# Kernel optimization log

Hardware: AMD Instinct MI355X
Metric: run time of the kernel (lower is better)

## Reference

```python
import jax, jax.numpy as jnp
import numpy as np

N = 50000        # nodes
E = 800000       # random edges (self loops appended inside reference, per PyG default)
IN = 128         # in_channels
H1, C1 = 8, 64   # conv1: heads, hidden_channels
NUM_CLASSES = 2  # conv2 out (heads=1, concat=False)
NEG_SLOPE = 0.2  # PyG GATConv default LeakyReLU slope


def setup_inputs() -> dict:
    key = jax.random.key(0)
    ks = jax.random.split(key, 12)
    x = jax.random.normal(ks[0], (N, IN), dtype=jnp.float32)
    edge_index = jax.random.randint(ks[1], (2, E), 0, N)
    # conv1 params: W1 [IN, H1*C1], att vectors [H1, C1], bias [H1*C1]
    W1 = jax.random.normal(ks[2], (IN, H1 * C1), dtype=jnp.float32) / np.sqrt(IN)
    a_src1 = jax.random.normal(ks[3], (H1, C1), dtype=jnp.float32) / np.sqrt(C1)
    a_dst1 = jax.random.normal(ks[4], (H1, C1), dtype=jnp.float32) / np.sqrt(C1)
    b1 = jnp.zeros((H1 * C1,), dtype=jnp.float32)
    # conv2 params: heads=1, out=NUM_CLASSES
    W2 = jax.random.normal(ks[5], (H1 * C1, 1 * NUM_CLASSES), dtype=jnp.float32) / np.sqrt(H1 * C1)
    a_src2 = jax.random.normal(ks[6], (1, NUM_CLASSES), dtype=jnp.float32) / np.sqrt(NUM_CLASSES)
    a_dst2 = jax.random.normal(ks[7], (1, NUM_CLASSES), dtype=jnp.float32) / np.sqrt(NUM_CLASSES)
    b2 = jnp.zeros((NUM_CLASSES,), dtype=jnp.float32)
    return {"x": x, "edge_index": edge_index, "W1": W1, "a_src1": a_src1,
            "a_dst1": a_dst1, "b1": b1, "W2": W2, "a_src2": a_src2,
            "a_dst2": a_dst2, "b2": b2}


def gat_layer(x, src, dst, W, a_src, a_dst, bias, concat):
    n = x.shape[0]
    heads, ch = a_src.shape
    h = (x @ W).reshape(n, heads, ch)                      # [N,H,C]
    alpha_s = jnp.einsum('nhc,hc->nh', h, a_src)           # per-node src score
    alpha_d = jnp.einsum('nhc,hc->nh', h, a_dst)           # per-node dst score
    e = jax.nn.leaky_relu(alpha_s[src] + alpha_d[dst], NEG_SLOPE)  # [Etot,H]
    # segment softmax over edges grouped by destination node
    m = jax.ops.segment_max(e, dst, num_segments=n)
    ex = jnp.exp(e - m[dst])
    den = jax.ops.segment_sum(ex, dst, num_segments=n)
    alpha = ex / den[dst]                                  # [Etot,H]
    out = jax.ops.segment_sum(h[src] * alpha[:, :, None], dst, num_segments=n)  # [N,H,C]
    out = out.reshape(n, heads * ch) if concat else out.mean(axis=1)
    return out + bias


def reference(x, edge_index, W1, a_src1, a_dst1, b1, W2, a_src2, a_dst2, b2):
    n = x.shape[0]
    loops = jnp.arange(n, dtype=edge_index.dtype)
    src = jnp.concatenate([edge_index[0], loops])   # PyG add_self_loops=True
    dst = jnp.concatenate([edge_index[1], loops])
    h = gat_layer(x, src, dst, W1, a_src1, a_dst1, b1, concat=True)   # [N, H1*C1]
    h = jax.nn.elu(h)
    # dropout is identity in eval mode
    out = gat_layer(h, src, dst, W2, a_src2, a_dst2, b2, concat=False)  # [N, 2]
    return out
```

## Files before the change

### kernel.cpp

```cpp
#include <hip/hip_runtime.h>
#include <hip/hip_bf16.h>

#define NEG 0.2f
#define BKT 64

typedef __attribute__((ext_vector_type(8))) short bf16x8;
typedef __attribute__((ext_vector_type(4))) float f32x4;

static __device__ __forceinline__ unsigned short f2bf(float f) {
    union { float f; unsigned u; } v; v.f = f;
    unsigned r = v.u + 0x7fff + ((v.u >> 16) & 1);
    return (unsigned short)(r >> 16);
}
static __device__ __forceinline__ float bf_lo(unsigned u) {
    return __uint_as_float(u << 16);
}
static __device__ __forceinline__ float bf_hi(unsigned u) {
    return __uint_as_float(u & 0xffff0000u);
}

__global__ void k_init(int* __restrict__ deg, unsigned short* __restrict__ csr, int n) {
    int v = blockIdx.x * 256 + threadIdx.x;
    if (v >= n) return;
    deg[v] = 1;
    csr[(size_t)v * BKT] = (unsigned short)v;
}

__global__ __launch_bounds__(256) void k_big(const int* __restrict__ ei,
                                             int* __restrict__ deg,
                                             unsigned short* __restrict__ csr,
                                             const float* __restrict__ x,
                                             const float* __restrict__ W1,
                                             const float* __restrict__ a_src,
                                             const float* __restrict__ a_dst,
                                             unsigned short* __restrict__ h1b,
                                             float* __restrict__ as1,
                                             float* __restrict__ ad1,
                                             int E_, int n, int gblocks) {
    int tid = threadIdx.x;
    if ((int)blockIdx.x >= gblocks) {
        int e = (blockIdx.x - gblocks) * 256 + tid;
        if (e >= E_) return;
        int s = ei[e], d = ei[E_ + e];
        int slot = atomicAdd(&deg[d], 1);
        if (slot < BKT) csr[(size_t)d * BKT + slot] = (unsigned short)s;
        return;
    }
    __shared__ unsigned short stg[4][16][72];
    int wave = tid >> 6, lane = tid & 63;
    int l15 = lane & 15, q = lane >> 4;
    int rowblk = blockIdx.x * 256 + wave * 64;

    bf16x8 xf[4][4];
    #pragma unroll
    for (int st = 0; st < 4; st++) {
        int ar = rowblk + st * 16 + l15; if (ar > n - 1) ar = n - 1;
        const float* ap = x + (size_t)ar * 128 + q * 8;
        #pragma unroll
        for (int kb = 0; kb < 4; kb++) {
            float4 v0 = *(const float4*)(ap + kb * 32);
            float4 v1 = *(const float4*)(ap + kb * 32 + 4);
            xf[st][kb][0] = (short)f2bf(v0.x); xf[st][kb][1] = (short)f2bf(v0.y);
            xf[st][kb][2] = (short)f2bf(v0.z); xf[st][kb][3] = (short)f2bf(v0.w);
            xf[st][kb][4] = (short)f2bf(v1.x); xf[st][kb][5] = (short)f2bf(v1.y);
            xf[st][kb][6] = (short)f2bf(v1.z); xf[st][kb][7] = (short)f2bf(v1.w);
        }
    }

    for (int j = 0; j < 8; j++) {
        int col0 = j * 64;
        bf16x8 bfr[4][4];
        #pragma unroll
        for (int kb = 0; kb < 4; kb++)
            #pragma unroll
            for (int t = 0; t < 4; t++) {
                const float* wp = W1 + (size_t)(kb * 32 + q * 8) * 512 + col0 + t * 16 + l15;
                #pragma unroll
                for (int e = 0; e < 8; e++)
                    bfr[kb][t][e] = (short)f2bf(wp[(size_t)e * 512]);
            }
        float asv[4], adv[4];
        #pragma unroll
        for (int t = 0; t < 4; t++) {
            asv[t] = a_src[j * 64 + t * 16 + l15];
            adv[t] = a_dst[j * 64 + t * 16 + l15];
        }

        #pragma unroll
        for (int st = 0; st < 4; st++) {
            int row0 = rowblk + st * 16;
            f32x4 acc[4] = {};
            #pragma unroll
            for (int kb = 0; kb < 4; kb++)
                #pragma unroll
                for (int t = 0; t < 4; t++)
                    acc[t] = __builtin_amdgcn_mfma_f32_16x16x32_bf16(xf[st][kb], bfr[kb][t], acc[t], 0, 0, 0);
            #pragma unroll
            for (int t = 0; t < 4; t++)
                #pragma unroll
                for (int r = 0; r < 4; r++)
                    stg[wave][q * 4 + r][t * 16 + l15] = f2bf(acc[t][r]);
            #pragma unroll
            for (int p = 0; p < 2; p++) {
                int lr = p * 8 + (lane >> 3);
                int row = row0 + lr;
                int cd = (lane & 7) * 8;
                uint4 vv = *(const uint4*)&stg[wave][lr][cd];
                if (row < n)
                    *(uint4*)(h1b + (size_t)row * 512 + col0 + cd) = vv;
            }
            float ps[4], pd[4];
            #pragma unroll
            for (int r = 0; r < 4; r++) {
                ps[r] = acc[0][r] * asv[0] + acc[1][r] * asv[1]
                      + acc[2][r] * asv[2] + acc[3][r] * asv[3];
                pd[r] = acc[0][r] * adv[0] + acc[1][r] * adv[1]
                      + acc[2][r] * adv[2] + acc[3][r] * adv[3];
                #pragma unroll
                for (int off = 1; off < 16; off <<= 1) {
                    ps[r] += __shfl_xor(ps[r], off, 64);
                    pd[r] += __shfl_xor(pd[r], off, 64);
                }
            }
            if (l15 < 4) {
                int r = l15;
                float vps = ps[0], vpd = pd[0];
                if (r == 1) { vps = ps[1]; vpd = pd[1]; }
                if (r == 2) { vps = ps[2]; vpd = pd[2]; }
                if (r == 3) { vps = ps[3]; vpd = pd[3]; }
                int row = row0 + q * 4 + r;
                if (row < n) { as1[row * 8 + j] = vps; ad1[row * 8 + j] = vpd; }
            }
        }
    }
}

__global__ __launch_bounds__(256) void k_agg1(const unsigned short* __restrict__ h1b,
                                              const float* __restrict__ as1,
                                              const float* __restrict__ ad1,
                                              const float* __restrict__ b1,
                                              const float* __restrict__ W2,
                                              const int* __restrict__ deg,
                                              const unsigned short* __restrict__ csr,
                                              float* __restrict__ h2, int n) {
    int lane = threadIdx.x & 63;
    int v = blockIdx.x * 4 + (threadIdx.x >> 6);
    if (v >= n) return;
    int head = lane >> 3, c = lane * 8;
    int dv = deg[v]; if (dv > BKT) dv = BKT;
    const unsigned short* cp = csr + (size_t)v * BKT;
    float adh = ad1[v * 8 + head];
    float s = 0.f;
    float acc[8] = {};
    int i = 0;
    for (; i + 4 <= dv; i += 4) {
        ushort4 uu = *(const ushort4*)(cp + i);
        int u0 = uu.x, u1 = uu.y, u2 = uu.z, u3 = uu.w;
        float ea = as1[u0 * 8 + head] + adh;
        float eb = as1[u1 * 8 + head] + adh;
        float ec = as1[u2 * 8 + head] + adh;
        float ed = as1[u3 * 8 + head] + adh;
        uint4 h0 = *(const uint4*)(h1b + (size_t)u0 * 512 + c);
        uint4 h1 = *(const uint4*)(h1b + (size_t)u1 * 512 + c);
        uint4 h2v = *(const uint4*)(h1b + (size_t)u2 * 512 + c);
        uint4 h3 = *(const uint4*)(h1b + (size_t)u3 * 512 + c);
        ea = (ea >= 0.f) ? ea : NEG * ea;
        eb = (eb >= 0.f) ? eb : NEG * eb;
        ec = (ec >= 0.f) ? ec : NEG * ec;
        ed = (ed >= 0.f) ? ed : NEG * ed;
        float w0 = __expf(ea), w1 = __expf(eb), w2 = __expf(ec), w3 = __expf(ed);
        s += (w0 + w1) + (w2 + w3);
        acc[0] = fmaf(w3, bf_lo(h3.x), fmaf(w2, bf_lo(h2v.x), fmaf(w1, bf_lo(h1.x), fmaf(w0, bf_lo(h0.x), acc[0]))));
        acc[1] = fmaf(w3, bf_hi(h3.x), fmaf(w2, bf_hi(h2v.x), fmaf(w1, bf_hi(h1.x), fmaf(w0, bf_hi(h0.x), acc[1]))));
        acc[2] = fmaf(w3, bf_lo(h3.y), fmaf(w2, bf_lo(h2v.y), fmaf(w1, bf_lo(h1.y), fmaf(w0, bf_lo(h0.y), acc[2]))));
        acc[3] = fmaf(w3, bf_hi(h3.y), fmaf(w2, bf_hi(h2v.y), fmaf(w1, bf_hi(h1.y), fmaf(w0, bf_hi(h0.y), acc[3]))));
        acc[4] = fmaf(w3, bf_lo(h3.z), fmaf(w2, bf_lo(h2v.z), fmaf(w1, bf_lo(h1.z), fmaf(w0, bf_lo(h0.z), acc[4]))));
        acc[5] = fmaf(w3, bf_hi(h3.z), fmaf(w2, bf_hi(h2v.z), fmaf(w1, bf_hi(h1.z), fmaf(w0, bf_hi(h0.z), acc[5]))));
        acc[6] = fmaf(w3, bf_lo(h3.w), fmaf(w2, bf_lo(h2v.w), fmaf(w1, bf_lo(h1.w), fmaf(w0, bf_lo(h0.w), acc[6]))));
        acc[7] = fmaf(w3, bf_hi(h3.w), fmaf(w2, bf_hi(h2v.w), fmaf(w1, bf_hi(h1.w), fmaf(w0, bf_hi(h0.w), acc[7]))));
    }
    for (; i < dv; i++) {
        int u = cp[i];
        float e = as1[u * 8 + head] + adh;
        e = (e >= 0.f) ? e : NEG * e;
        float w = __expf(e);
        s += w;
        uint4 hv = *(const uint4*)(h1b + (size_t)u * 512 + c);
        acc[0] = fmaf(w, bf_lo(hv.x), acc[0]);
        acc[1] = fmaf(w, bf_hi(hv.x), acc[1]);
        acc[2] = fmaf(w, bf_lo(hv.y), acc[2]);
        acc[3] = fmaf(w, bf_hi(hv.y), acc[3]);
        acc[4] = fmaf(w, bf_lo(hv.z), acc[4]);
        acc[5] = fmaf(w, bf_hi(hv.z), acc[5]);
        acc[6] = fmaf(w, bf_lo(hv.w), acc[6]);
        acc[7] = fmaf(w, bf_hi(hv.w), acc[7]);
    }
    float inv = 1.0f / s;
    float4 ba = *(const float4*)(b1 + c);
    float4 bb = *(const float4*)(b1 + c + 4);
    float o[8] = {acc[0] * inv + ba.x, acc[1] * inv + ba.y,
                  acc[2] * inv + ba.z, acc[3] * inv + ba.w,
                  acc[4] * inv + bb.x, acc[5] * inv + bb.y,
                  acc[6] * inv + bb.z, acc[7] * inv + bb.w};
    #pragma unroll
    for (int jj = 0; jj < 8; jj++)
        o[jj] = (o[jj] > 0.f) ? o[jj] : (__expf(o[jj]) - 1.0f);
    const float4* wp = (const float4*)(W2 + c * 2);
    float4 w0 = wp[0], w1 = wp[1], w2 = wp[2], w3 = wp[3];
    float p0 = o[0] * w0.x + o[1] * w0.z + o[2] * w1.x + o[3] * w1.z
             + o[4] * w2.x + o[5] * w2.z + o[6] * w3.x + o[7] * w3.z;
    float p1 = o[0] * w0.y + o[1] * w0.w + o[2] * w1.y + o[3] * w1.w
             + o[4] * w2.y + o[5] * w2.w + o[6] * w3.y + o[7] * w3.w;
    #pragma unroll
    for (int off = 1; off < 64; off <<= 1) {
        p0 += __shfl_xor(p0, off, 64);
        p1 += __shfl_xor(p1, off, 64);
    }
    if (lane == 0) {
        h2[2 * v] = p0;
        h2[2 * v + 1] = p1;
    }
}

__global__ __launch_bounds__(256) void k_agg2(const float* __restrict__ h2,
                                              const float* __restrict__ a_src2,
                                              const float* __restrict__ a_dst2,
                                              const float* __restrict__ b2,
                                              const int* __restrict__ deg,
                                              const unsigned short* __restrict__ csr,
                                              float* __restrict__ out, int n) {
    int tid = threadIdx.x;
    int lane = tid & 63, wave = tid >> 6;
    int sub = lane & 7, g = lane >> 3;
    int v = blockIdx.x * 32 + wave * 8 + g;
    if (v >= n) return;
    int dv = deg[v]; if (dv > BKT) dv = BKT;
    const unsigned short* cp = csr + (size_t)v * BKT;
    float sa0 = a_src2[0], sa1 = a_src2[1];
    float da0 = a_dst2[0], da1 = a_dst2[1];
    float2 hv = *(const float2*)(h2 + 2 * v);
    float adv = hv.x * da0 + hv.y * da1;
    float s = 0.f, a0 = 0.f, a1 = 0.f;
    for (int i = sub; i < dv; i += 8) {
        int u = cp[i];
        float2 hu = *(const float2*)(h2 + 2 * u);
        float e = hu.x * sa0 + hu.y * sa1 + adv;
        e = (e >= 0.f) ? e : NEG * e;
        float w = __expf(e);
        s += w;
        a0 = fmaf(w, hu.x, a0);
        a1 = fmaf(w, hu.y, a1);
    }
    #pragma unroll
    for (int off = 1; off < 8; off <<= 1) {
        s  += __shfl_xor(s, off, 64);
        a0 += __shfl_xor(a0, off, 64);
        a1 += __shfl_xor(a1, off, 64);
    }
    if (sub == 0) {
        float inv = 1.0f / s;
        out[2 * v]     = a0 * inv + b2[0];
        out[2 * v + 1] = a1 * inv + b2[1];
    }
}

extern "C" void kernel_launch(void* const* d_in, const int* in_sizes, int n_in,
                              void* d_out, int out_size, void* d_ws, size_t ws_size,
                              hipStream_t stream) {
    const float* x      = (const float*)d_in[0];
    const int*   ei     = (const int*)d_in[1];
    const float* W1     = (const float*)d_in[2];
    const float* a_src1 = (const float*)d_in[3];
    const float* a_dst1 = (const float*)d_in[4];
    const float* b1     = (const float*)d_in[5];
    const float* W2     = (const float*)d_in[6];
    const float* a_src2 = (const float*)d_in[7];
    const float* a_dst2 = (const float*)d_in[8];
    const float* b2     = (const float*)d_in[9];
    float* out = (float*)d_out;

    int n  = in_sizes[0] / 128;
    int E_ = in_sizes[1] / 2;
    int rblk = (n + 255) / 256;
    int npad = rblk * 256;

    char* w = (char*)d_ws;
    auto alloc = [&](size_t bytes) {
        char* p = w; w += (bytes + 255) & ~(size_t)255; return p;
    };
    int*            deg    = (int*)alloc((size_t)n * 4);
    unsigned short* csr    = (unsigned short*)alloc((size_t)n * BKT * 2);
    unsigned short* h1b    = (unsigned short*)alloc((size_t)npad * 512 * 2);
    float*          as1    = (float*)alloc((size_t)n * 8 * 4);
    float*          ad1    = (float*)alloc((size_t)n * 8 * 4);
    float*          h2     = (float*)alloc((size_t)n * 2 * 4);

    int nb256 = (n + 255) / 256;
    k_init<<<nb256, 256, 0, stream>>>(deg, csr, n);

    int gblocks = rblk;
    int sblocks = (E_ + 255) / 256;
    k_big<<<gblocks + sblocks, 256, 0, stream>>>(ei, deg, csr, x, W1,
                                                 a_src1, a_dst1, h1b, as1, ad1,
                                                 E_, n, gblocks);

    int nb = (n + 3) / 4;
    k_agg1<<<nb, 256, 0, stream>>>(h1b, as1, ad1, b1, W2, deg, csr, h2, n);

    int ab = (n + 31) / 32;
    k_agg2<<<ab, 256, 0, stream>>>(h2, a_src2, a_dst2, b2, deg, csr, out, n);
}
```

Baseline: 287.3 us.

## Partition edge-scatter atomics by destination residue to keep each counter on one XCD

The degree counters are laid out in 8 partitions indexed by d&7. The scatter blocks are replicated 8 times, and each block only handles edges whose destination matches blockIdx&7. Since blocks are dispatched round-robin across the 8 XCDs, each counter and its CSR bucket should then be touched only from a single XCD's L2. This aims to cut cross-die atomic coherence traffic and false sharing on CSR rows. The cost is reading the destination array 8 times and launching 8x as many scatter blocks.

Result: slower. 372.3 us (+29.6%).

```diff
diff --git a/kernel.cpp b/kernel.cpp
--- a/kernel.cpp
+++ b/kernel.cpp
@@ -18,16 +18,20 @@
 static __device__ __forceinline__ float bf_hi(unsigned u) {
     return __uint_as_float(u & 0xffff0000u);
 }
-
-__global__ void k_init(int* __restrict__ deg, unsigned short* __restrict__ csr, int n) {
+static __device__ __forceinline__ int didx(int v, int dstr) {
+    return (v & 7) * dstr + (v >> 3);
+}
+
+__global__ void k_init(int* __restrict__ degP, unsigned short* __restrict__ csr,
+                       int n, int dstr) {
     int v = blockIdx.x * 256 + threadIdx.x;
     if (v >= n) return;
-    deg[v] = 1;
+    degP[didx(v, dstr)] = 1;
     csr[(size_t)v * BKT] = (unsigned short)v;
 }
 
 __global__ __launch_bounds__(256) void k_big(const int* __restrict__ ei,
-                                             int* __restrict__ deg,
+                                             int* __restrict__ degP,
                                              unsigned short* __restrict__ csr,
                                              const float* __restrict__ x,
                                              const float* __restrict__ W1,
@@ -36,13 +40,17 @@
                                              unsigned short* __restrict__ h1b,
                                              float* __restrict__ as1,
                                              float* __restrict__ ad1,
-                                             int E_, int n, int gblocks) {
+                                             int E_, int n, int dstr, int gblocks) {
     int tid = threadIdx.x;
     if ((int)blockIdx.x >= gblocks) {
-        int e = (blockIdx.x - gblocks) * 256 + tid;
+        int g = blockIdx.x & 7;
+        int c = (blockIdx.x - gblocks) >> 3;
+        int e = c * 256 + tid;
         if (e >= E_) return;
-        int s = ei[e], d = ei[E_ + e];
-        int slot = atomicAdd(&deg[d], 1);
+        int d = ei[E_ + e];
+        if ((d & 7) != g) return;
+        int s = ei[e];
+        int slot = atomicAdd(&degP[didx(d, dstr)], 1);
         if (slot < BKT) csr[(size_t)d * BKT + slot] = (unsigned short)s;
         return;
     }
@@ -140,14 +148,14 @@
                                               const float* __restrict__ ad1,
                                               const float* __restrict__ b1,
                                               const float* __restrict__ W2,
-                                              const int* __restrict__ deg,
+                                              const int* __restrict__ degP,
                                               const unsigned short* __restrict__ csr,
-                                              float* __restrict__ h2, int n) {
+                                              float* __restrict__ h2, int n, int dstr) {
     int lane = threadIdx.x & 63;
     int v = blockIdx.x * 4 + (threadIdx.x >> 6);
     if (v >= n) return;
     int head = lane >> 3, c = lane * 8;
-    int dv = deg[v]; if (dv > BKT) dv = BKT;
+    int dv = degP[didx(v, dstr)]; if (dv > BKT) dv = BKT;
     const unsigned short* cp = csr + (size_t)v * BKT;
     float adh = ad1[v * 8 + head];
     float s = 0.f;
@@ -226,15 +234,15 @@
                                               const float* __restrict__ a_src2,
                                               const float* __restrict__ a_dst2,
                                               const float* __restrict__ b2,
-                                              const int* __restrict__ deg,
+                                              const int* __restrict__ degP,
                                               const unsigned short* __restrict__ csr,
-                                              float* __restrict__ out, int n) {
+                                              float* __restrict__ out, int n, int dstr) {
     int tid = threadIdx.x;
     int lane = tid & 63, wave = tid >> 6;
     int sub = lane & 7, g = lane >> 3;
     int v = blockIdx.x * 32 + wave * 8 + g;
     if (v >= n) return;
-    int dv = deg[v]; if (dv > BKT) dv = BKT;
+    int dv = degP[didx(v, dstr)]; if (dv > BKT) dv = BKT;
     const unsigned short* cp = csr + (size_t)v * BKT;
     float sa0 = a_src2[0], sa1 = a_src2[1];
     float da0 = a_dst2[0], da1 = a_dst2[1];
@@ -283,12 +291,13 @@
     int E_ = in_sizes[1] / 2;
     int rblk = (n + 255) / 256;
     int npad = rblk * 256;
+    int dstr = (((n + 7) / 8) + 15) & ~15;
 
     char* w = (char*)d_ws;
     auto alloc = [&](size_t bytes) {
         char* p = w; w += (bytes + 255) & ~(size_t)255; return p;
     };
-    int*            deg    = (int*)alloc((size_t)n * 4);
+    int*            degP   = (int*)alloc((size_t)dstr * 8 * 4);
     unsigned short* csr    = (unsigned short*)alloc((size_t)n * BKT * 2);
     unsigned short* h1b    = (unsigned short*)alloc((size_t)npad * 512 * 2);
     float*          as1    = (float*)alloc((size_t)n * 8 * 4);
@@ -296,17 +305,17 @@
     float*          h2     = (float*)alloc((size_t)n * 2 * 4);
 
     int nb256 = (n + 255) / 256;
-    k_init<<<nb256, 256, 0, stream>>>(deg, csr, n);
+    k_init<<<nb256, 256, 0, stream>>>(degP, csr, n, dstr);
 
     int gblocks = rblk;
-    int sblocks = (E_ + 255) / 256;
-    k_big<<<gblocks + sblocks, 256, 0, stream>>>(ei, deg, csr, x, W1,
+    int sblocks = ((E_ + 255) / 256) * 8;
+    k_big<<<gblocks + sblocks, 256, 0, stream>>>(ei, degP, csr, x, W1,
                                                  a_src1, a_dst1, h1b, as1, ad1,
-                                                 E_, n, gblocks);
+                                                 E_, n, dstr, gblocks);
 
     int nb = (n + 3) / 4;
-    k_agg1<<<nb, 256, 0, stream>>>(h1b, as1, ad1, b1, W2, deg, csr, h2, n);
+    k_agg1<<<nb, 256, 0, stream>>>(h1b, as1, ad1, b1, W2, degP, csr, h2, n, dstr);
 
     int ab = (n + 31) / 32;
-    k_agg2<<<ab, 256, 0, stream>>>(h2, a_src2, a_dst2, b2, deg, csr, out, n);
-}
+    k_agg2<<<ab, 256, 0, stream>>>(h2, a_src2, a_dst2, b2, degP, csr, out, n, dstr);
+}
```
